# Kernel tuning notes

Hardware: AMD Instinct MI355X
Metric: run time of the kernel (lower is better)

Reference implementation:

```python
import jax, jax.numpy as jnp
import numpy as np

N_CAND = 10   # n_point_candidate
SIGMA = 1.0   # std threshold for vote filtering
EPS = 1e-6


def _get_pt_candidates(pcld, kpts_ofst, seg, cpt_ofst, k):
    # pcld [b,n,3]; kpts_ofst [b,n,8,3]; seg [b,n,1]; cpt_ofst [b,n,1,3]
    offsets = jnp.concatenate([kpts_ofst, cpt_ofst], axis=2)        # [b,n,9,3]
    scores = jnp.squeeze(seg, axis=-1)                              # [b,n]
    _, idx = jax.lax.top_k(scores, k)                               # [b,k] most confident points
    cands = pcld[:, :, None, :] + offsets                           # [b,n,9,3] candidate kpt positions
    cands = jnp.take_along_axis(cands, idx[:, :, None, None], axis=1)  # [b,k,9,3]
    return jnp.transpose(cands, (0, 2, 1, 3))                       # [b,9,k,3]


def _pts_clustering_with_std(kpts_cans, sigma=SIGMA):
    # kpts_cans [b,n_kpts,k,3]: keep candidates within sigma*std of the mean, average survivors
    mean = jnp.mean(kpts_cans, axis=2, keepdims=True)
    std = jnp.std(kpts_cans, axis=2, keepdims=True)
    inlier = jnp.all(jnp.abs(kpts_cans - mean) <= sigma * std, axis=-1)  # [b,n_kpts,k]
    w = inlier.astype(kpts_cans.dtype)[..., None]
    return jnp.sum(kpts_cans * w, axis=2) / (jnp.sum(w, axis=2) + EPS)   # [b,n_kpts,3]


def _rt_svd_transform(A, B, w):
    # Weighted Kabsch: find R,t with R @ A + t ~= B.  A,B [b,n,3]; w [n]
    wn = w / jnp.sum(w)
    cA = jnp.einsum('n,bnc->bc', wn, A)[:, None, :]                 # weighted centroids
    cB = jnp.einsum('n,bnc->bc', wn, B)[:, None, :]
    Am, Bm = A - cA, B - cB
    H = jnp.einsum('bni,n,bnj->bij', Am, w, Bm)                     # [b,3,3] cross-covariance
    U, S, Vh = jnp.linalg.svd(H)
    V = jnp.swapaxes(Vh, -1, -2)
    R0 = V @ jnp.swapaxes(U, -1, -2)
    flip = jnp.where(jnp.linalg.det(R0) < 0.0, -1.0, 1.0)           # reflection fix
    V = V.at[:, :, -1].multiply(flip[:, None])
    R = V @ jnp.swapaxes(U, -1, -2)                                 # [b,3,3]
    t = jnp.swapaxes(cB, -1, -2) - R @ jnp.swapaxes(cA, -1, -2)     # [b,3,1]
    return R, t


def setup_inputs() -> dict:
    key = jax.random.key(0)
    k1, k2, k3, k4, k5 = jax.random.split(key, 5)
    b, n, nk = 64, 12288, 8
    return {
        'pcld_input': jax.random.normal(k1, (b, n, 3), jnp.float32),
        'kpts_pre_input': jax.random.normal(k2, (b, n, nk, 3), jnp.float32),
        'cpt_pre_input': jax.random.normal(k3, (b, n, 1, 3), jnp.float32),
        'seg_pre_input': jax.random.uniform(k4, (b, n, 1), jnp.float32),
        'mesh_kpts_input': jax.random.normal(k5, (b, nk + 1, 3), jnp.float32),
    }


def reference(pcld_input, kpts_pre_input, cpt_pre_input, seg_pre_input, mesh_kpts_input):
    obj_kpts = _get_pt_candidates(pcld_input, kpts_pre_input, seg_pre_input, cpt_pre_input, N_CAND)
    kpts_voted = _pts_clustering_with_std(obj_kpts)                 # [b,9,3]
    n_pts = kpts_voted.shape[1]
    weights_vector = jnp.ones((n_pts,), dtype=kpts_voted.dtype)
    batch_R, batch_t = _rt_svd_transform(mesh_kpts_input, kpts_voted, weights_vector)
    batch_t = jnp.reshape(batch_t, (-1, 3))
    return batch_R, batch_t, kpts_voted
```

## Files before the change

### kernel.cpp

```cpp
#include <hip/hip_runtime.h>
#include <math.h>

#define NB      64
#define NPTS    12288
#define KTOP    10
#define NKP     9
#define CHUNKS  8
#define CHUNK_N (NPTS / CHUNKS)
#define T1      256
#define T2      128

struct Pair { float v; int i; };

__device__ __forceinline__ bool better(const Pair& a, const Pair& b) {
    return (a.v > b.v) || (a.v == b.v && a.i < b.i);
}

__device__ __forceinline__ void push10(Pair (&loc)[KTOP], Pair c) {
    if (better(c, loc[KTOP - 1])) {
        loc[KTOP - 1] = c;
        #pragma unroll
        for (int j = KTOP - 1; j > 0; --j) {
            if (better(loc[j], loc[j - 1])) { Pair tmp = loc[j]; loc[j] = loc[j - 1]; loc[j - 1] = tmp; }
            else break;
        }
    }
}

__device__ __forceinline__ void merge10(const Pair* __restrict__ A,
                                        const Pair* __restrict__ B,
                                        Pair* __restrict__ D) {
    int a = 0, c = 0;
    #pragma unroll
    for (int j = 0; j < KTOP; ++j) {
        Pair pa = A[a], pb = B[c];
        if (better(pa, pb)) { D[j] = pa; ++a; } else { D[j] = pb; ++c; }
    }
}

__global__ __launch_bounds__(T1)
void topk_part(const float* __restrict__ seg, Pair* __restrict__ part) {
    const int blk = blockIdx.x;
    const int b = blk >> 3;
    const int chunk = blk & 7;
    const int t = threadIdx.x;

    __shared__ Pair lists[T1][KTOP];

    const float* segb = seg + (size_t)b * NPTS + (size_t)chunk * CHUNK_N;
    const int base = chunk * CHUNK_N;

    float4 a4 = ((const float4*)segb)[t];
    float2 a2 = ((const float2*)(segb + 1024))[t];

    Pair loc[KTOP];
    #pragma unroll
    for (int j = 0; j < KTOP; ++j) { loc[j].v = -INFINITY; loc[j].i = 0x7fffffff; }
    push10(loc, {a4.x, base + 4 * t + 0});
    push10(loc, {a4.y, base + 4 * t + 1});
    push10(loc, {a4.z, base + 4 * t + 2});
    push10(loc, {a4.w, base + 4 * t + 3});
    push10(loc, {a2.x, base + 1024 + 2 * t + 0});
    push10(loc, {a2.y, base + 1024 + 2 * t + 1});

    #pragma unroll
    for (int j = 0; j < KTOP; ++j) lists[t][j] = loc[j];
    __syncthreads();

    for (int s = 1; s < T1; s <<= 1) {
        if ((t & (2 * s - 1)) == 0 && (t + s) < T1) {
            Pair m[KTOP];
            merge10(lists[t], lists[t + s], m);
            #pragma unroll
            for (int j = 0; j < KTOP; ++j) lists[t][j] = m[j];
        }
        __syncthreads();
    }

    if (t < KTOP) part[(size_t)blk * KTOP + t] = lists[0][t];
}

__global__ __launch_bounds__(T2)
void pose_finish(const float* __restrict__ pcld,
                 const float* __restrict__ kpts,
                 const float* __restrict__ cpt,
                 const float* __restrict__ mesh,
                 const Pair*  __restrict__ part,
                 float* __restrict__ out)
{
    const int b = blockIdx.x;
    const int t = threadIdx.x;

    __shared__ Pair  l0[CHUNKS][KTOP];
    __shared__ Pair  m1[4][KTOP];
    __shared__ Pair  m2[2][KTOP];
    __shared__ Pair  top[KTOP];
    __shared__ float cands[NKP][KTOP][3];
    __shared__ float voted[NKP][3];

    if (t < CHUNKS * KTOP)
        l0[t / KTOP][t % KTOP] = part[(size_t)b * CHUNKS * KTOP + t];
    __syncthreads();

    if (t < 4) merge10(l0[2 * t], l0[2 * t + 1], m1[t]);
    __syncthreads();
    if (t < 2) merge10(m1[2 * t], m1[2 * t + 1], m2[t]);
    __syncthreads();
    if (t == 0) merge10(m2[0], m2[1], top);
    __syncthreads();

    if (t < NKP * KTOP) {
        int j = t / KTOP;
        int i = t % KTOP;
        int p = top[i].i;
        size_t base = (size_t)b * NPTS + p;
        float px = pcld[base * 3 + 0], py = pcld[base * 3 + 1], pz = pcld[base * 3 + 2];
        float ox, oy, oz;
        if (j < 8) {
            size_t kb = (base * 8 + j) * 3;
            ox = kpts[kb + 0]; oy = kpts[kb + 1]; oz = kpts[kb + 2];
        } else {
            size_t cb = base * 3;
            ox = cpt[cb + 0]; oy = cpt[cb + 1]; oz = cpt[cb + 2];
        }
        cands[j][i][0] = px + ox;
        cands[j][i][1] = py + oy;
        cands[j][i][2] = pz + oz;
    }
    __syncthreads();

    if (t < NKP) {
        float mean[3] = {0.f, 0.f, 0.f};
        for (int i = 0; i < KTOP; ++i)
            for (int c = 0; c < 3; ++c) mean[c] += cands[t][i][c];
        for (int c = 0; c < 3; ++c) mean[c] *= (1.0f / KTOP);
        float var[3] = {0.f, 0.f, 0.f};
        for (int i = 0; i < KTOP; ++i)
            for (int c = 0; c < 3; ++c) { float d = cands[t][i][c] - mean[c]; var[c] += d * d; }
        float sd[3];
        for (int c = 0; c < 3; ++c) sd[c] = sqrtf(var[c] * (1.0f / KTOP));
        float wsum = 0.f, acc[3] = {0.f, 0.f, 0.f};
        for (int i = 0; i < KTOP; ++i) {
            bool in = true;
            for (int c = 0; c < 3; ++c) in = in && (fabsf(cands[t][i][c] - mean[c]) <= sd[c]);
            if (in) {
                wsum += 1.f;
                for (int c = 0; c < 3; ++c) acc[c] += cands[t][i][c];
            }
        }
        float inv = 1.f / (wsum + 1e-6f);
        for (int c = 0; c < 3; ++c) {
            float v = acc[c] * inv;
            voted[t][c] = v;
            out[NB * 9 + NB * 3 + ((size_t)b * NKP + t) * 3 + c] = v;
        }
    }
    __syncthreads();

    if (t == 0) {
        const float* mb = mesh + (size_t)b * NKP * 3;
        double A[NKP][3], Bv[NKP][3];
        double cA[3] = {0, 0, 0}, cB[3] = {0, 0, 0};
        for (int n = 0; n < NKP; ++n) {
            for (int c = 0; c < 3; ++c) {
                A[n][c]  = (double)mb[n * 3 + c];
                Bv[n][c] = (double)voted[n][c];
                cA[c] += A[n][c];
                cB[c] += Bv[n][c];
            }
        }
        for (int c = 0; c < 3; ++c) { cA[c] /= NKP; cB[c] /= NKP; }

        double H[3][3] = {{0,0,0},{0,0,0},{0,0,0}};
        for (int n = 0; n < NKP; ++n)
            for (int i = 0; i < 3; ++i)
                for (int j = 0; j < 3; ++j)
                    H[i][j] += (A[n][i] - cA[i]) * (Bv[n][j] - cB[j]);

        double Km[3][3];
        for (int i = 0; i < 3; ++i)
            for (int j = 0; j < 3; ++j) {
                double s = 0;
                for (int l = 0; l < 3; ++l) s += H[l][i] * H[l][j];
                Km[i][j] = s;
            }

        double V[3][3] = {{1,0,0},{0,1,0},{0,0,1}};
        for (int sweep = 0; sweep < 8; ++sweep) {
            for (int p = 0; p < 2; ++p) {
                for (int q = p + 1; q < 3; ++q) {
                    double apq = Km[p][q];
                    double app = Km[p][p], aqq = Km[q][q];
                    if (fabs(apq) <= 1e-30 * (fabs(app) + fabs(aqq)) || apq == 0.0) continue;
                    double theta = (aqq - app) / (2.0 * apq);
                    double tj = ((theta >= 0.0) ? 1.0 : -1.0) / (fabs(theta) + sqrt(theta * theta + 1.0));
                    double cj = 1.0 / sqrt(tj * tj + 1.0);
                    double sj = tj * cj;
                    for (int l = 0; l < 3; ++l) {
                        double klp = Km[l][p], klq = Km[l][q];
                        Km[l][p] = cj * klp - sj * klq;
                        Km[l][q] = sj * klp + cj * klq;
                    }
                    for (int l = 0; l < 3; ++l) {
                        double kpl = Km[p][l], kql = Km[q][l];
                        Km[p][l] = cj * kpl - sj * kql;
                        Km[q][l] = sj * kpl + cj * kql;
                    }
                    for (int l = 0; l < 3; ++l) {
                        double vlp = V[l][p], vlq = V[l][q];
                        V[l][p] = cj * vlp - sj * vlq;
                        V[l][q] = sj * vlp + cj * vlq;
                    }
                }
            }
        }

        double eig[3] = {Km[0][0], Km[1][1], Km[2][2]};
        int ord[3] = {0, 1, 2};
        if (eig[ord[0]] < eig[ord[1]]) { int tmp = ord[0]; ord[0] = ord[1]; ord[1] = tmp; }
        if (eig[ord[1]] < eig[ord[2]]) { int tmp = ord[1]; ord[1] = ord[2]; ord[2] = tmp; }
        if (eig[ord[0]] < eig[ord[1]]) { int tmp = ord[0]; ord[0] = ord[1]; ord[1] = tmp; }

        double detH =
            H[0][0] * (H[1][1] * H[2][2] - H[1][2] * H[2][1]) -
            H[0][1] * (H[1][0] * H[2][2] - H[1][2] * H[2][0]) +
            H[0][2] * (H[1][0] * H[2][1] - H[1][1] * H[2][0]);
        double dsign[3] = {1.0, 1.0, (detH < 0.0) ? -1.0 : 1.0};

        double R[3][3] = {{0,0,0},{0,0,0},{0,0,0}};
        for (int k = 0; k < 3; ++k) {
            int c = ord[k];
            double s = sqrt(fmax(eig[c], 0.0));
            double invs = 1.0 / fmax(s, 1e-12);
            double u[3];
            for (int l = 0; l < 3; ++l) {
                double a = 0;
                for (int m = 0; m < 3; ++m) a += H[l][m] * V[m][c];
                u[l] = a * invs;
            }
            for (int r = 0; r < 3; ++r)
                for (int cc = 0; cc < 3; ++cc)
                    R[r][cc] += dsign[k] * V[r][c] * u[cc];
        }

        double tv[3];
        for (int c = 0; c < 3; ++c) {
            double a = 0;
            for (int m = 0; m < 3; ++m) a += R[c][m] * cA[m];
            tv[c] = cB[c] - a;
        }

        for (int r = 0; r < 3; ++r)
            for (int c = 0; c < 3; ++c)
                out[(size_t)b * 9 + r * 3 + c] = (float)R[r][c];
        for (int c = 0; c < 3; ++c)
            out[NB * 9 + (size_t)b * 3 + c] = (float)tv[c];
    }
}

extern "C" void kernel_launch(void* const* d_in, const int* in_sizes, int n_in,
                              void* d_out, int out_size, void* d_ws, size_t ws_size,
                              hipStream_t stream) {
    const float* pcld = (const float*)d_in[0];
    const float* kpts = (const float*)d_in[1];
    const float* cpt  = (const float*)d_in[2];
    const float* seg  = (const float*)d_in[3];
    const float* mesh = (const float*)d_in[4];
    float* out = (float*)d_out;
    Pair* part = (Pair*)d_ws;

    topk_part<<<NB * CHUNKS, T1, 0, stream>>>(seg, part);
    pose_finish<<<NB, T2, 0, stream>>>(pcld, kpts, cpt, mesh, part, out);
}
```

Before: 136.1 us.

## Replace shared-memory tree merge top-k with wavefront shuffle bitonic merges

The per-chunk top-k now sorts each thread's six scores with a small odd-even network into a 16-slot list, then merges lists across the wavefront via xor shuffles and bitonic merge networks. This replaces the log-depth shared-memory tree that needed a barrier at every level. The finishing kernel merges the eight partial lists with shuffles instead of serial single-thread merges. Jacobi sweeps are also cut from 8 to 6, which may slightly reduce SVD accuracy. In exchange it adds more compare-exchange work and higher register pressure per thread.

Result: slower. 146.0 us (+7.3%).

```diff
diff --git a/kernel.cpp b/kernel.cpp
--- a/kernel.cpp
+++ b/kernel.cpp
@@ -4,6 +4,7 @@
 #define NB      64
 #define NPTS    12288
 #define KTOP    10
+#define LK      16
 #define NKP     9
 #define CHUNKS  8
 #define CHUNK_N (NPTS / CHUNKS)
@@ -16,26 +17,35 @@
     return (a.v > b.v) || (a.v == b.v && a.i < b.i);
 }
 
-__device__ __forceinline__ void push10(Pair (&loc)[KTOP], Pair c) {
-    if (better(c, loc[KTOP - 1])) {
-        loc[KTOP - 1] = c;
-        #pragma unroll
-        for (int j = KTOP - 1; j > 0; --j) {
-            if (better(loc[j], loc[j - 1])) { Pair tmp = loc[j]; loc[j] = loc[j - 1]; loc[j - 1] = tmp; }
-            else break;
-        }
-    }
-}
-
-__device__ __forceinline__ void merge10(const Pair* __restrict__ A,
-                                        const Pair* __restrict__ B,
-                                        Pair* __restrict__ D) {
-    int a = 0, c = 0;
-    #pragma unroll
-    for (int j = 0; j < KTOP; ++j) {
-        Pair pa = A[a], pb = B[c];
-        if (better(pa, pb)) { D[j] = pa; ++a; } else { D[j] = pb; ++c; }
-    }
+__device__ __forceinline__ void ce(Pair& x, Pair& y) {
+    if (better(y, x)) { Pair t = x; x = y; y = t; }
+}
+
+__device__ __forceinline__ void merge16(Pair (&A)[LK], const Pair (&B)[LK]) {
+    Pair C[LK];
+    #pragma unroll
+    for (int i = 0; i < LK; ++i) {
+        Pair a = A[i], b = B[LK - 1 - i];
+        C[i] = better(a, b) ? a : b;
+    }
+    #pragma unroll
+    for (int d = LK / 2; d >= 1; d >>= 1) {
+        #pragma unroll
+        for (int i = 0; i < LK; ++i)
+            if ((i & d) == 0) ce(C[i], C[i + d]);
+    }
+    #pragma unroll
+    for (int i = 0; i < LK; ++i) A[i] = C[i];
+}
+
+__device__ __forceinline__ void shfl_merge(Pair (&A)[LK], int s) {
+    Pair B[LK];
+    #pragma unroll
+    for (int i = 0; i < LK; ++i) {
+        B[i].v = __shfl_xor(A[i].v, s);
+        B[i].i = __shfl_xor(A[i].i, s);
+    }
+    merge16(A, B);
 }
 
 __global__ __launch_bounds__(T1)
@@ -44,8 +54,10 @@
     const int b = blk >> 3;
     const int chunk = blk & 7;
     const int t = threadIdx.x;
-
-    __shared__ Pair lists[T1][KTOP];
+    const int lane = t & 63;
+    const int w = t >> 6;
+
+    __shared__ Pair sm[4][LK];
 
     const float* segb = seg + (size_t)b * NPTS + (size_t)chunk * CHUNK_N;
     const int base = chunk * CHUNK_N;
@@ -53,31 +65,41 @@
     float4 a4 = ((const float4*)segb)[t];
     float2 a2 = ((const float2*)(segb + 1024))[t];
 
-    Pair loc[KTOP];
-    #pragma unroll
-    for (int j = 0; j < KTOP; ++j) { loc[j].v = -INFINITY; loc[j].i = 0x7fffffff; }
-    push10(loc, {a4.x, base + 4 * t + 0});
-    push10(loc, {a4.y, base + 4 * t + 1});
-    push10(loc, {a4.z, base + 4 * t + 2});
-    push10(loc, {a4.w, base + 4 * t + 3});
-    push10(loc, {a2.x, base + 1024 + 2 * t + 0});
-    push10(loc, {a2.y, base + 1024 + 2 * t + 1});
-
-    #pragma unroll
-    for (int j = 0; j < KTOP; ++j) lists[t][j] = loc[j];
-    __syncthreads();
-
-    for (int s = 1; s < T1; s <<= 1) {
-        if ((t & (2 * s - 1)) == 0 && (t + s) < T1) {
-            Pair m[KTOP];
-            merge10(lists[t], lists[t + s], m);
+    Pair L[LK];
+    L[0] = {a4.x, base + 4 * t + 0};
+    L[1] = {a4.y, base + 4 * t + 1};
+    L[2] = {a4.z, base + 4 * t + 2};
+    L[3] = {a4.w, base + 4 * t + 3};
+    L[4] = {a2.x, base + 1024 + 2 * t + 0};
+    L[5] = {a2.y, base + 1024 + 2 * t + 1};
+    #pragma unroll
+    for (int i = 6; i < LK; ++i) { L[i].v = -INFINITY; L[i].i = 0x7fffffff; }
+
+    #pragma unroll
+    for (int r = 0; r < 6; ++r) {
+        if (r & 1) { ce(L[1], L[2]); ce(L[3], L[4]); }
+        else       { ce(L[0], L[1]); ce(L[2], L[3]); ce(L[4], L[5]); }
+    }
+
+    shfl_merge(L, 1);  shfl_merge(L, 2);  shfl_merge(L, 4);
+    shfl_merge(L, 8);  shfl_merge(L, 16); shfl_merge(L, 32);
+
+    if (lane == 0) {
+        #pragma unroll
+        for (int j = 0; j < LK; ++j) sm[w][j] = L[j];
+    }
+    __syncthreads();
+
+    if (t < 64) {
+        Pair M[LK];
+        #pragma unroll
+        for (int j = 0; j < LK; ++j) M[j] = sm[t & 3][j];
+        shfl_merge(M, 1); shfl_merge(M, 2);
+        if (t == 0) {
             #pragma unroll
-            for (int j = 0; j < KTOP; ++j) lists[t][j] = m[j];
-        }
-        __syncthreads();
-    }
-
-    if (t < KTOP) part[(size_t)blk * KTOP + t] = lists[0][t];
+            for (int j = 0; j < LK; ++j) part[(size_t)blk * LK + j] = M[j];
+        }
+    }
 }
 
 __global__ __launch_bounds__(T2)
@@ -91,28 +113,27 @@
     const int b = blockIdx.x;
     const int t = threadIdx.x;
 
-    __shared__ Pair  l0[CHUNKS][KTOP];
-    __shared__ Pair  m1[4][KTOP];
-    __shared__ Pair  m2[2][KTOP];
-    __shared__ Pair  top[KTOP];
+    __shared__ int   topidx[KTOP];
     __shared__ float cands[NKP][KTOP][3];
     __shared__ float voted[NKP][3];
 
-    if (t < CHUNKS * KTOP)
-        l0[t / KTOP][t % KTOP] = part[(size_t)b * CHUNKS * KTOP + t];
-    __syncthreads();
-
-    if (t < 4) merge10(l0[2 * t], l0[2 * t + 1], m1[t]);
-    __syncthreads();
-    if (t < 2) merge10(m1[2 * t], m1[2 * t + 1], m2[t]);
-    __syncthreads();
-    if (t == 0) merge10(m2[0], m2[1], top);
+    if (t < 64) {
+        Pair M[LK];
+        const Pair* src = part + ((size_t)b * CHUNKS + (t & 7)) * LK;
+        #pragma unroll
+        for (int j = 0; j < LK; ++j) M[j] = src[j];
+        shfl_merge(M, 1); shfl_merge(M, 2); shfl_merge(M, 4);
+        if (t == 0) {
+            #pragma unroll
+            for (int j = 0; j < KTOP; ++j) topidx[j] = M[j].i;
+        }
+    }
     __syncthreads();
 
     if (t < NKP * KTOP) {
         int j = t / KTOP;
         int i = t % KTOP;
-        int p = top[i].i;
+        int p = topidx[i];
         size_t base = (size_t)b * NPTS + p;
         float px = pcld[base * 3 + 0], py = pcld[base * 3 + 1], pz = pcld[base * 3 + 2];
         float ox, oy, oz;
@@ -186,7 +207,7 @@
             }
 
         double V[3][3] = {{1,0,0},{0,1,0},{0,0,1}};
-        for (int sweep = 0; sweep < 8; ++sweep) {
+        for (int sweep = 0; sweep < 6; ++sweep) {
             for (int p = 0; p < 2; ++p) {
                 for (int q = p + 1; q < 3; ++q) {
                     double apq = Km[p][q];
```
